# Kernel tuning notes

Measured on AMD Instinct MI355X. Metric: run time of the kernel, lower is better.

## Reference

```python
import jax, jax.numpy as jnp
import numpy as np

HEADS = 16
D_MODEL = 1024


def setup_inputs() -> dict:
    key = jax.random.key(0)
    ks = jax.random.split(key, 12)
    B, S, D = 4, 2048, D_MODEL
    s = 1.0 / np.sqrt(D)
    return {
        "q": jax.random.normal(ks[0], (B, S, D), jnp.float32),
        "k": jax.random.normal(ks[1], (B, S, D), jnp.float32),
        "v": jax.random.normal(ks[2], (B, S, D), jnp.float32),
        "mask": jnp.ones((B, S, S), jnp.int32),
        "W_q": jax.random.normal(ks[3], (D, D), jnp.float32) * s,
        "b_q": jnp.zeros((D,), jnp.float32),
        "W_k": jax.random.normal(ks[4], (D, D), jnp.float32) * s,
        "b_k": jnp.zeros((D,), jnp.float32),
        "W_v": jax.random.normal(ks[5], (D, D), jnp.float32) * s,
        "b_v": jnp.zeros((D,), jnp.float32),
        "W_o": jax.random.normal(ks[6], (D, D), jnp.float32) * s,
        "b_o": jnp.zeros((D,), jnp.float32),
    }


def reference(q, k, v, mask, W_q, b_q, W_k, b_k, W_v, b_v, W_o, b_o):
    B, Sq, D = q.shape
    H = HEADS
    d_k = D // H
    # torch Linear: x @ W.T + b
    qh = (q @ W_q.T + b_q).reshape(B, Sq, H, d_k).transpose(0, 2, 1, 3)
    kh = (k @ W_k.T + b_k).reshape(B, -1, H, d_k).transpose(0, 2, 1, 3)
    vh = (v @ W_v.T + b_v).reshape(B, -1, H, d_k).transpose(0, 2, 1, 3)
    scores = jnp.einsum("bhqd,bhkd->bhqk", qh, kh) / jnp.sqrt(jnp.float32(d_k))
    scores = jnp.where(mask[:, None, :, :] == 0, -jnp.inf, scores)
    attn = jax.nn.softmax(scores, axis=-1)
    out = jnp.einsum("bhqk,bhkd->bhqd", attn, vh)
    out = out.transpose(0, 2, 1, 3).reshape(B, Sq, D)
    return out @ W_o.T + b_o
```

## Files before the change

### kernel.cpp

```cpp
#include <hip/hip_runtime.h>
#include <hip/hip_bf16.h>
#include <cmath>
#include <cstddef>

#define B_  4
#define S_  2048
#define D_  1024
#define H_  16
#define DK_ 64
#define M_  (B_*S_)
#define MB(x) ((size_t)(x) << 20)

typedef unsigned short u16;
typedef __attribute__((ext_vector_type(8))) short s16x8;
typedef __attribute__((ext_vector_type(8))) unsigned short u16x8;
typedef __attribute__((ext_vector_type(4))) unsigned short u16x4;
typedef __attribute__((ext_vector_type(4))) float f32x4;
typedef __attribute__((ext_vector_type(4))) unsigned int u32x4;
typedef __attribute__((ext_vector_type(2))) unsigned long long ull2;

typedef __attribute__((address_space(3))) char as3char;
typedef __attribute__((address_space(1))) const char as1char;

__device__ inline u16 f2bf(float f) {
  unsigned int u = __float_as_uint(f);
  u += 0x7fffu + ((u >> 16) & 1u);
  return (u16)(u >> 16);
}
__device__ inline float bf2f(u16 h) {
  return __uint_as_float(((unsigned int)h) << 16);
}

__global__ __launch_bounds__(256)
void pack_mask(const int* __restrict__ mask, unsigned long long* __restrict__ Mp)
{
  int w    = blockIdx.x * 4 + (threadIdx.x >> 6);
  int lane = threadIdx.x & 63;
  int m = mask[(size_t)w * 64 + lane];
  unsigned long long bits = __ballot(m != 0);
  if (lane == 0) Mp[w] = bits;
}

__global__ __launch_bounds__(256)
void split_w(const float* __restrict__ W, u16* __restrict__ hi,
             u16* __restrict__ lo)
{
  int i = (blockIdx.x * 256 + threadIdx.x) * 4;
  float4 x = *(const float4*)(W + i);
  float xs[4] = {x.x, x.y, x.z, x.w};
  u16x4 h, l;
#pragma unroll
  for (int e = 0; e < 4; ++e) {
    u16 hh = f2bf(xs[e]);
    h[e] = hh;
    l[e] = f2bf(xs[e] - bf2f(hh));
  }
  *(u16x4*)(hi + i) = h;
  *(u16x4*)(lo + i) = l;
}

__global__ __launch_bounds__(256)
void cvt3(const float* __restrict__ a, const float* __restrict__ b,
          const float* __restrict__ c, u16* __restrict__ oa,
          u16* __restrict__ ob, u16* __restrict__ oc)
{
  const float* src = blockIdx.z == 0 ? a : (blockIdx.z == 1 ? b : c);
  u16*         dst = blockIdx.z == 0 ? oa : (blockIdx.z == 1 ? ob : oc);
  int id = blockIdx.x * 256 + threadIdx.x;
  int m  = id >> 7;
  int k8 = (id & 127) << 3;
  const float* p = src + (size_t)m * 1024 + k8;
  float4 x0 = *(const float4*)p;
  float4 x1 = *(const float4*)(p + 4);
  u16x8 px;
  px[0]=f2bf(x0.x); px[1]=f2bf(x0.y); px[2]=f2bf(x0.z); px[3]=f2bf(x0.w);
  px[4]=f2bf(x1.x); px[5]=f2bf(x1.y); px[6]=f2bf(x1.z); px[7]=f2bf(x1.w);
  int row = m & 127, kk = k8 & 63;
  size_t byte = ((size_t)((m >> 7) * 16 + (k8 >> 6)) << 14)
              + (size_t)((row * 128 + (kk >> 3) * 16) ^ ((row & 7) << 4));
  *(u16x8*)((char*)dst + byte) = px;
}

template<int OH, int ODK>
__global__ __launch_bounds__(256)
void proj_gemm_t(const u16* __restrict__ Xb, const u16* __restrict__ Wb,
                 const float* __restrict__ bias, u16* __restrict__ out,
                 float scale)
{
  __shared__ __align__(16) u16 smem[16384];
  char* const sX = (char*)smem;
  char* const sW = (char*)smem + 16384;

  const int tid  = threadIdx.x;
  const int lane = tid & 63, wid = tid >> 6;
  const int l15  = lane & 15, l4 = lane >> 4;
  const int wm = (wid >> 1) * 64, wn = (wid & 1) * 64;
  const int mb = blockIdx.x, nb = blockIdx.y;

  f32x4 acc[4][4];
#pragma unroll
  for (int i = 0; i < 4; ++i)
#pragma unroll
    for (int j = 0; j < 4; ++j)
      acc[i][j] = f32x4{0.f, 0.f, 0.f, 0.f};

  const char* xsrc = (const char*)Xb + ((size_t)(mb * 16) << 14) + wid * 4096 + lane * 16;
  const char* wsrc = (const char*)Wb + ((size_t)(nb * 16) << 14) + wid * 4096 + lane * 16;

  for (int kb = 0; kb < 16; ++kb) {
#pragma unroll
    for (int i = 0; i < 4; ++i) {
      __builtin_amdgcn_global_load_lds((const as1char*)(xsrc + i * 1024),
                                       (as3char*)(sX + wid * 4096 + i * 1024), 16, 0, 0);
      __builtin_amdgcn_global_load_lds((const as1char*)(wsrc + i * 1024),
                                       (as3char*)(sW + wid * 4096 + i * 1024), 16, 0, 0);
    }
    xsrc += 16384; wsrc += 16384;
    __syncthreads();

#pragma unroll
    for (int kc = 0; kc < 2; ++kc) {
      s16x8 af[4], bf[4];
#pragma unroll
      for (int i = 0; i < 4; ++i) {
        int ar = wm + i * 16 + l15;
        af[i] = *(const s16x8*)(sX + ((ar * 128 + kc * 64 + l4 * 16) ^ ((ar & 7) << 4)));
        int br = wn + i * 16 + l15;
        bf[i] = *(const s16x8*)(sW + ((br * 128 + kc * 64 + l4 * 16) ^ ((br & 7) << 4)));
      }
#pragma unroll
      for (int i = 0; i < 4; ++i)
#pragma unroll
        for (int j = 0; j < 4; ++j)
          acc[i][j] = __builtin_amdgcn_mfma_f32_16x16x32_bf16(af[i], bf[j], acc[i][j], 0, 0, 0);
    }
    __syncthreads();
  }

  float bj[4];
#pragma unroll
  for (int j = 0; j < 4; ++j) bj[j] = bias[nb * 128 + wn + j * 16 + l15];

#pragma unroll
  for (int i = 0; i < 4; ++i) {
#pragma unroll
    for (int r = 0; r < 4; ++r) {
      int mm = mb * 128 + wm + i * 16 + l4 * 4 + r;
      int bb = mm >> 11, s = mm & (S_ - 1);
#pragma unroll
      for (int j = 0; j < 4; ++j) {
        int n = nb * 128 + wn + j * 16 + l15;
        int hh = n / ODK, d = n % ODK;
        out[(((size_t)bb * OH + hh) * S_ + s) * ODK + d] =
            f2bf((acc[i][j][r] + bj[j]) * scale);
      }
    }
  }
}

__global__ __launch_bounds__(256)
void proj_out_split(const u16* __restrict__ Xhi, const u16* __restrict__ Xlo,
                    const u16* __restrict__ Whi, const u16* __restrict__ Wlo,
                    const float* __restrict__ bias, float* __restrict__ out,
                    int M, int N, int K)
{
  __shared__ __align__(16) u16 smem[32768];
  char* const sXh = (char*)smem;
  char* const sXl = (char*)smem + 16384;
  char* const sWh = (char*)smem + 32768;
  char* const sWl = (char*)smem + 49152;

  const int tid  = threadIdx.x;
  const int lane = tid & 63, wid = tid >> 6;
  const int l15  = lane & 15, l4 = lane >> 4;
  const int wm = (wid >> 1) * 64, wn = (wid & 1) * 64;
  const int m0 = blockIdx.x * 128, n0 = blockIdx.y * 128;

  f32x4 acc[4][4];
#pragma unroll
  for (int i = 0; i < 4; ++i)
#pragma unroll
    for (int j = 0; j < 4; ++j)
      acc[i][j] = f32x4{0.f, 0.f, 0.f, 0.f};

  for (int k0 = 0; k0 < K; k0 += 64) {
    __syncthreads();
#pragma unroll
    for (int n = 0; n < 4; ++n) {
      int c   = tid + n * 256;
      int row = c >> 3;
      int k8  = (c & 7) * 8;
      int dst = (row * 128 + (c & 7) * 16) ^ ((row & 7) << 4);
      size_t xoff = (size_t)(m0 + row) * K + k0 + k8;
      size_t woff = (size_t)(n0 + row) * K + k0 + k8;
      *(u16x8*)(sXh + dst) = *(const u16x8*)(Xhi + xoff);
      *(u16x8*)(sXl + dst) = *(const u16x8*)(Xlo + xoff);
      *(u16x8*)(sWh + dst) = *(const u16x8*)(Whi + woff);
      *(u16x8*)(sWl + dst) = *(const u16x8*)(Wlo + woff);
    }
    __syncthreads();

#pragma unroll
    for (int kc = 0; kc < 2; ++kc) {
      s16x8 ah[4], al[4], bh[4], bl[4];
#pragma unroll
      for (int i = 0; i < 4; ++i) {
        int ar = wm + i * 16 + l15;
        int aoff = (ar * 128 + kc * 64 + l4 * 16) ^ ((ar & 7) << 4);
        ah[i] = *(const s16x8*)(sXh + aoff);
        al[i] = *(const s16x8*)(sXl + aoff);
        int br = wn + i * 16 + l15;
        int boff = (br * 128 + kc * 64 + l4 * 16) ^ ((br & 7) << 4);
        bh[i] = *(const s16x8*)(sWh + boff);
        bl[i] = *(const s16x8*)(sWl + boff);
      }
#pragma unroll
      for (int i = 0; i < 4; ++i)
#pragma unroll
        for (int j = 0; j < 4; ++j) {
          acc[i][j] = __builtin_amdgcn_mfma_f32_16x16x32_bf16(ah[i], bh[j], acc[i][j], 0, 0, 0);
          acc[i][j] = __builtin_amdgcn_mfma_f32_16x16x32_bf16(ah[i], bl[j], acc[i][j], 0, 0, 0);
          acc[i][j] = __builtin_amdgcn_mfma_f32_16x16x32_bf16(al[i], bh[j], acc[i][j], 0, 0, 0);
        }
    }
  }

  float bj[4];
#pragma unroll
  for (int j = 0; j < 4; ++j) bj[j] = bias[n0 + wn + j * 16 + l15];

#pragma unroll
  for (int i = 0; i < 4; ++i) {
#pragma unroll
    for (int r = 0; r < 4; ++r) {
      int mm = m0 + wm + i * 16 + l4 * 4 + r;
#pragma unroll
      for (int j = 0; j < 4; ++j) {
        int n = n0 + wn + j * 16 + l15;
        out[(size_t)mm * N + n] = acc[i][j][r] + bj[j];
      }
    }
  }
}

__global__ __launch_bounds__(512)
void flash_attn_mfma4(const u16* __restrict__ Qh, const u16* __restrict__ Kh,
                      const u16* __restrict__ Vh,
                      const unsigned long long* __restrict__ Mp,
                      u16* __restrict__ AOhi, u16* __restrict__ AOlo)
{
  __shared__ __align__(16) char smem[16896];
  char* const sK = smem;
  char* const sV = smem + 8192;

  const int tid  = threadIdx.x;
  const int lane = tid & 63, wid = tid >> 6;
  const int l15  = lane & 15, l4 = lane >> 4;

  const int bh = blockIdx.y;
  const int b  = bh >> 4, h = bh & 15;
  const int q0 = blockIdx.x * 128;
  const int qw = q0 + wid * 16;
  const int myq = qw + l15;

  const float L2E = 1.4426950408889634f;

  const u16* qbase = Qh + ((size_t)bh * S_ + myq) * DK_;
  s16x8 qf[2];
  qf[0] = *(const s16x8*)(qbase + l4 * 8);
  qf[1] = *(const s16x8*)(qbase + 32 + l4 * 8);

  const int srow = tid >> 3;
  const int sd8  = (tid & 7) * 8;
  const int kdst = (srow * 128 + (tid & 7) * 16) ^ ((srow & 7) << 4);
  const u16* kg = Kh + (size_t)bh * S_ * DK_ + (size_t)srow * DK_ + sd8;
  const u16* vg = Vh + (size_t)bh * S_ * DK_ + (size_t)srow * DK_ + sd8;

  const int kswz = (l15 & 7) << 4;
  const int kcol = l4 * 16;

  const unsigned long long* mrow = Mp + ((size_t)b * S_ + myq) * (S_ / 64);

  f32x4 o[4];
#pragma unroll
  for (int n = 0; n < 4; ++n) o[n] = f32x4{0.f, 0.f, 0.f, 0.f};
  float m_i = -INFINITY, l_i = 0.f;
  float ml2 = -1e30f * L2E;

  for (int t = 0; t < S_ / 64; ++t) {
    __syncthreads();
    *(u16x8*)(sK + kdst) = *(const u16x8*)(kg + (size_t)t * 64 * DK_);
    u16x8 vv = *(const u16x8*)(vg + (size_t)t * 64 * DK_);
#pragma unroll
    for (int e = 0; e < 8; ++e) {
      int d = sd8 + e;
      *(u16*)(sV + d * 136 + ((srow * 2) ^ (((d >> 3) & 7) << 4))) = (u16)vv[e];
    }
    unsigned long long mbits = mrow[t];
    __syncthreads();

    f32x4 sc[4];
#pragma unroll
    for (int n = 0; n < 4; ++n) {
      sc[n] = f32x4{0.f, 0.f, 0.f, 0.f};
#pragma unroll
      for (int kc = 0; kc < 2; ++kc) {
        int row = n * 16 + l15;
        s16x8 kf = *(const s16x8*)(sK + ((row * 128 + kc * 64 + kcol) ^ kswz));
        sc[n] = __builtin_amdgcn_mfma_f32_16x16x32_bf16(kf, qf[kc], sc[n], 0, 0, 0);
      }
    }

    float s[4][4];
    if (__all(mbits == 0xFFFFFFFFFFFFFFFFull)) {
#pragma unroll
      for (int n = 0; n < 4; ++n)
#pragma unroll
        for (int r = 0; r < 4; ++r) s[n][r] = sc[n][r];
    } else {
#pragma unroll
      for (int n = 0; n < 4; ++n) {
        unsigned mb2 = (unsigned)(mbits >> (n * 16 + l4 * 4)) & 15u;
#pragma unroll
        for (int r = 0; r < 4; ++r)
          s[n][r] = (mb2 >> r) & 1u ? sc[n][r] : -INFINITY;
      }
    }

    float mt = fmaxf(fmaxf(s[0][0], s[0][1]), fmaxf(s[0][2], s[0][3]));
#pragma unroll
    for (int n = 1; n < 4; ++n)
      mt = fmaxf(mt, fmaxf(fmaxf(s[n][0], s[n][1]), fmaxf(s[n][2], s[n][3])));
    mt = fmaxf(mt, __shfl_xor(mt, 16));
    mt = fmaxf(mt, __shfl_xor(mt, 32));

    if (!__all(mt - m_i <= 8.f)) {
      float mn = fmaxf(m_i, mt);
      float alpha = (m_i == -INFINITY) ? 0.f
                    : __builtin_amdgcn_exp2f((m_i - mn) * L2E);
      float ab[4];
#pragma unroll
      for (int r = 0; r < 4; ++r) ab[r] = __shfl(alpha, l4 * 4 + r);
#pragma unroll
      for (int n = 0; n < 4; ++n)
#pragma unroll
        for (int r = 0; r < 4; ++r) o[n][r] *= ab[r];
      l_i *= alpha;
      m_i = mn;
      ml2 = fmaxf(mn, -1e30f) * L2E;
    }

    float p[4][4];
    float rs = 0.f;
#pragma unroll
    for (int n = 0; n < 4; ++n)
#pragma unroll
      for (int r = 0; r < 4; ++r) {
        p[n][r] = __builtin_amdgcn_exp2f(fmaf(s[n][r], L2E, -ml2));
        rs += p[n][r];
      }
    rs += __shfl_xor(rs, 16);
    rs += __shfl_xor(rs, 32);
    l_i += rs;

    s16x8 pf[2];
#pragma unroll
    for (int kc = 0; kc < 2; ++kc) {
      unsigned r0, r1, r2, r3;
      asm("v_cvt_pk_bf16_f32 %0, %1, %2" : "=v"(r0) : "v"(p[2*kc][0]),   "v"(p[2*kc][1]));
      asm("v_cvt_pk_bf16_f32 %0, %1, %2" : "=v"(r1) : "v"(p[2*kc][2]),   "v"(p[2*kc][3]));
      asm("v_cvt_pk_bf16_f32 %0, %1, %2" : "=v"(r2) : "v"(p[2*kc+1][0]), "v"(p[2*kc+1][1]));
      asm("v_cvt_pk_bf16_f32 %0, %1, %2" : "=v"(r3) : "v"(p[2*kc+1][2]), "v"(p[2*kc+1][3]));
      u32x4 uu = {r0, r1, r2, r3};
      pf[kc] = __builtin_bit_cast(s16x8, uu);
    }

#pragma unroll
    for (int kc = 0; kc < 2; ++kc) {
      int k0b = kc * 64 + 8 * l4;
#pragma unroll
      for (int n = 0; n < 4; ++n) {
        int d    = n * 16 + l15;
        int rowb = d * 136;
        int swz  = ((d >> 3) & 7) << 4;
        ull2 uu;
        uu[0] = *(const unsigned long long*)(sV + rowb + (k0b ^ swz));
        uu[1] = *(const unsigned long long*)(sV + rowb + ((k0b + 32) ^ swz));
        s16x8 vf = __builtin_bit_cast(s16x8, uu);
        o[n] = __builtin_amdgcn_mfma_f32_16x16x32_bf16(pf[kc], vf, o[n], 0, 0, 0);
      }
    }
  }

  float linv[4];
#pragma unroll
  for (int r = 0; r < 4; ++r) {
    float lr = __shfl(l_i, l4 * 4 + r);
    linv[r] = lr > 0.f ? 1.f / lr : 0.f;
  }
#pragma unroll
  for (int n = 0; n < 4; ++n)
#pragma unroll
    for (int r = 0; r < 4; ++r) {
      float val = o[n][r] * linv[r];
      u16 hh = f2bf(val);
      size_t oa = ((size_t)b * S_ + qw + l4 * 4 + r) * D_ + h * 64 + n * 16 + l15;
      AOhi[oa] = hh;
      AOlo[oa] = f2bf(val - bf2f(hh));
    }
}

extern "C" void kernel_launch(void* const* d_in, const int* in_sizes, int n_in,
                              void* d_out, int out_size, void* d_ws, size_t ws_size,
                              hipStream_t stream)
{
  const float* q    = (const float*)d_in[0];
  const float* k    = (const float*)d_in[1];
  const float* v    = (const float*)d_in[2];
  const int*   mask = (const int*)  d_in[3];
  const float* Wq   = (const float*)d_in[4];
  const float* bq   = (const float*)d_in[5];
  const float* Wk   = (const float*)d_in[6];
  const float* bk   = (const float*)d_in[7];
  const float* Wv   = (const float*)d_in[8];
  const float* bv   = (const float*)d_in[9];
  const float* Wo   = (const float*)d_in[10];
  const float* bo   = (const float*)d_in[11];
  float* out = (float*)d_out;

  char* ws = (char*)d_ws;
  u16* Qh   = (u16*)(ws);
  u16* Kh   = (u16*)(ws + MB(16));
  u16* Vh   = (u16*)(ws + MB(32));
  u16* AOhi = (u16*)(ws + MB(48));
  u16* AOlo = (u16*)(ws + MB(64));
  u16* Whi  = (u16*)(ws + MB(80));
  u16* Wlo  = (u16*)(ws + MB(82));
  unsigned long long* Mp = (unsigned long long*)(ws + MB(84));
  u16* kb2  = (u16*)(ws + MB(48));
  u16* qb2  = (u16*)(ws + MB(64));
  u16* vb2  = (u16*)(ws + MB(86));
  u16* Wqb  = (u16*)(ws + MB(102));
  u16* Wkb  = (u16*)(ws + MB(104));
  u16* Wvb  = (u16*)(ws + MB(106));

  dim3 tblk(256);

  cvt3<<<dim3(4096, 1, 3), tblk, 0, stream>>>(q, k, v, qb2, kb2, vb2);
  cvt3<<<dim3(512, 1, 3), tblk, 0, stream>>>(Wq, Wk, Wv, Wqb, Wkb, Wvb);
  pack_mask<<<dim3((B_ * S_ * (S_ / 64)) / 4), tblk, 0, stream>>>(mask, Mp);
  split_w<<<dim3((D_ * D_) / 1024), tblk, 0, stream>>>(Wo, Whi, Wlo);

  dim3 gproj(M_ / 128, D_ / 128);
  proj_gemm_t<H_, DK_><<<gproj, tblk, 0, stream>>>(qb2, Wqb, bq, Qh, 0.125f);
  proj_gemm_t<H_, DK_><<<gproj, tblk, 0, stream>>>(kb2, Wkb, bk, Kh, 1.0f);
  proj_gemm_t<H_, DK_><<<gproj, tblk, 0, stream>>>(vb2, Wvb, bv, Vh, 1.0f);

  dim3 gattn(S_ / 128, B_ * H_);
  flash_attn_mfma4<<<gattn, dim3(512), 0, stream>>>(Qh, Kh, Vh, Mp, AOhi, AOlo);

  proj_out_split<<<gproj, tblk, 0, stream>>>(AOhi, AOlo, Whi, Wlo, bo, out,
                                             M_, D_, D_);
}
```

Baseline: 317.3 us.

## Pre-tile operands, transpose V, and prefetch K/V tiles in attention

The V projection now writes a head-transposed layout (d-major), so the attention kernel can store V into shared memory with one vector write per thread instead of eight scalar transposing writes. The attention kernel also register-prefetches the next K/V tile and mask word. The attention output and the split Wo are written in the pre-swizzled tiled layout, so the output projection can load tiles straight into LDS with global_load_lds. The cost is scattered 2-byte stores in the attention epilogue and the V projection epilogue, plus an extra barrier per k-step in the output GEMM.

Result: faster. 301.1 us (-5.1%).

```diff
diff --git a/kernel.cpp b/kernel.cpp
--- a/kernel.cpp
+++ b/kernel.cpp
@@ -31,6 +31,12 @@
   return __uint_as_float(((unsigned int)h) << 16);
 }
 
+__device__ inline size_t tsw(int m, int k) {
+  int row = m & 127, kk = k & 63;
+  return ((size_t)((m >> 7) * 16 + (k >> 6)) << 14)
+       + (size_t)(((row * 128 + (kk >> 3) * 16) ^ ((row & 7) << 4)) + (kk & 7) * 2);
+}
+
 __global__ __launch_bounds__(256)
 void pack_mask(const int* __restrict__ mask, unsigned long long* __restrict__ Mp)
 {
@@ -42,21 +48,26 @@
 }
 
 __global__ __launch_bounds__(256)
-void split_w(const float* __restrict__ W, u16* __restrict__ hi,
-             u16* __restrict__ lo)
-{
-  int i = (blockIdx.x * 256 + threadIdx.x) * 4;
-  float4 x = *(const float4*)(W + i);
-  float xs[4] = {x.x, x.y, x.z, x.w};
-  u16x4 h, l;
-#pragma unroll
-  for (int e = 0; e < 4; ++e) {
+void split_w_t(const float* __restrict__ W, u16* __restrict__ hi,
+               u16* __restrict__ lo)
+{
+  int id = blockIdx.x * 256 + threadIdx.x;
+  int n  = id >> 7;
+  int k8 = (id & 127) << 3;
+  const float* p = W + (size_t)n * 1024 + k8;
+  float4 x0 = *(const float4*)p;
+  float4 x1 = *(const float4*)(p + 4);
+  float xs[8] = {x0.x, x0.y, x0.z, x0.w, x1.x, x1.y, x1.z, x1.w};
+  u16x8 h, l;
+#pragma unroll
+  for (int e = 0; e < 8; ++e) {
     u16 hh = f2bf(xs[e]);
     h[e] = hh;
     l[e] = f2bf(xs[e] - bf2f(hh));
   }
-  *(u16x4*)(hi + i) = h;
-  *(u16x4*)(lo + i) = l;
+  size_t byte = tsw(n, k8);
+  *(u16x8*)((char*)hi + byte) = h;
+  *(u16x8*)((char*)lo + byte) = l;
 }
 
 __global__ __launch_bounds__(256)
@@ -75,13 +86,10 @@
   u16x8 px;
   px[0]=f2bf(x0.x); px[1]=f2bf(x0.y); px[2]=f2bf(x0.z); px[3]=f2bf(x0.w);
   px[4]=f2bf(x1.x); px[5]=f2bf(x1.y); px[6]=f2bf(x1.z); px[7]=f2bf(x1.w);
-  int row = m & 127, kk = k8 & 63;
-  size_t byte = ((size_t)((m >> 7) * 16 + (k8 >> 6)) << 14)
-              + (size_t)((row * 128 + (kk >> 3) * 16) ^ ((row & 7) << 4));
-  *(u16x8*)((char*)dst + byte) = px;
-}
-
-template<int OH, int ODK>
+  *(u16x8*)((char*)dst + tsw(m, k8)) = px;
+}
+
+template<int MODE>
 __global__ __launch_bounds__(256)
 void proj_gemm_t(const u16* __restrict__ Xb, const u16* __restrict__ Wb,
                  const float* __restrict__ bias, u16* __restrict__ out,
@@ -150,19 +158,21 @@
 #pragma unroll
       for (int j = 0; j < 4; ++j) {
         int n = nb * 128 + wn + j * 16 + l15;
-        int hh = n / ODK, d = n % ODK;
-        out[(((size_t)bb * OH + hh) * S_ + s) * ODK + d] =
-            f2bf((acc[i][j][r] + bj[j]) * scale);
+        int hh = n >> 6, d = n & 63;
+        u16 val = f2bf((acc[i][j][r] + bj[j]) * scale);
+        if (MODE == 0)
+          out[(((size_t)bb * H_ + hh) * S_ + s) * DK_ + d] = val;
+        else
+          out[(((size_t)bb * H_ + hh) * DK_ + d) * S_ + s] = val;
       }
     }
   }
 }
 
 __global__ __launch_bounds__(256)
-void proj_out_split(const u16* __restrict__ Xhi, const u16* __restrict__ Xlo,
-                    const u16* __restrict__ Whi, const u16* __restrict__ Wlo,
-                    const float* __restrict__ bias, float* __restrict__ out,
-                    int M, int N, int K)
+void proj_out_t(const u16* __restrict__ Xhi, const u16* __restrict__ Xlo,
+                const u16* __restrict__ Whi, const u16* __restrict__ Wlo,
+                const float* __restrict__ bias, float* __restrict__ out)
 {
   __shared__ __align__(16) u16 smem[32768];
   char* const sXh = (char*)smem;
@@ -174,7 +184,7 @@
   const int lane = tid & 63, wid = tid >> 6;
   const int l15  = lane & 15, l4 = lane >> 4;
   const int wm = (wid >> 1) * 64, wn = (wid & 1) * 64;
-  const int m0 = blockIdx.x * 128, n0 = blockIdx.y * 128;
+  const int mb = blockIdx.x, nb = blockIdx.y;
 
   f32x4 acc[4][4];
 #pragma unroll
@@ -183,21 +193,25 @@
     for (int j = 0; j < 4; ++j)
       acc[i][j] = f32x4{0.f, 0.f, 0.f, 0.f};
 
-  for (int k0 = 0; k0 < K; k0 += 64) {
-    __syncthreads();
-#pragma unroll
-    for (int n = 0; n < 4; ++n) {
-      int c   = tid + n * 256;
-      int row = c >> 3;
-      int k8  = (c & 7) * 8;
-      int dst = (row * 128 + (c & 7) * 16) ^ ((row & 7) << 4);
-      size_t xoff = (size_t)(m0 + row) * K + k0 + k8;
-      size_t woff = (size_t)(n0 + row) * K + k0 + k8;
-      *(u16x8*)(sXh + dst) = *(const u16x8*)(Xhi + xoff);
-      *(u16x8*)(sXl + dst) = *(const u16x8*)(Xlo + xoff);
-      *(u16x8*)(sWh + dst) = *(const u16x8*)(Whi + woff);
-      *(u16x8*)(sWl + dst) = *(const u16x8*)(Wlo + woff);
-    }
+  const int toff = wid * 4096 + lane * 16;
+  const char* xh = (const char*)Xhi + ((size_t)(mb * 16) << 14) + toff;
+  const char* xl = (const char*)Xlo + ((size_t)(mb * 16) << 14) + toff;
+  const char* wh = (const char*)Whi + ((size_t)(nb * 16) << 14) + toff;
+  const char* wl = (const char*)Wlo + ((size_t)(nb * 16) << 14) + toff;
+
+  for (int kb = 0; kb < 16; ++kb) {
+#pragma unroll
+    for (int i = 0; i < 4; ++i) {
+      __builtin_amdgcn_global_load_lds((const as1char*)(xh + i * 1024),
+                                       (as3char*)(sXh + wid * 4096 + i * 1024), 16, 0, 0);
+      __builtin_amdgcn_global_load_lds((const as1char*)(xl + i * 1024),
+                                       (as3char*)(sXl + wid * 4096 + i * 1024), 16, 0, 0);
+      __builtin_amdgcn_global_load_lds((const as1char*)(wh + i * 1024),
+                                       (as3char*)(sWh + wid * 4096 + i * 1024), 16, 0, 0);
+      __builtin_amdgcn_global_load_lds((const as1char*)(wl + i * 1024),
+                                       (as3char*)(sWl + wid * 4096 + i * 1024), 16, 0, 0);
+    }
+    xh += 16384; xl += 16384; wh += 16384; wl += 16384;
     __syncthreads();
 
 #pragma unroll
@@ -223,29 +237,30 @@
           acc[i][j] = __builtin_amdgcn_mfma_f32_16x16x32_bf16(al[i], bh[j], acc[i][j], 0, 0, 0);
         }
     }
+    __syncthreads();
   }
 
   float bj[4];
 #pragma unroll
-  for (int j = 0; j < 4; ++j) bj[j] = bias[n0 + wn + j * 16 + l15];
+  for (int j = 0; j < 4; ++j) bj[j] = bias[nb * 128 + wn + j * 16 + l15];
 
 #pragma unroll
   for (int i = 0; i < 4; ++i) {
 #pragma unroll
     for (int r = 0; r < 4; ++r) {
-      int mm = m0 + wm + i * 16 + l4 * 4 + r;
+      int mm = mb * 128 + wm + i * 16 + l4 * 4 + r;
 #pragma unroll
       for (int j = 0; j < 4; ++j) {
-        int n = n0 + wn + j * 16 + l15;
-        out[(size_t)mm * N + n] = acc[i][j][r] + bj[j];
+        int n = nb * 128 + wn + j * 16 + l15;
+        out[(size_t)mm * D_ + n] = acc[i][j][r] + bj[j];
       }
     }
   }
 }
 
 __global__ __launch_bounds__(512)
-void flash_attn_mfma4(const u16* __restrict__ Qh, const u16* __restrict__ Kh,
-                      const u16* __restrict__ Vh,
+void flash_attn_mfma5(const u16* __restrict__ Qh, const u16* __restrict__ Kh,
+                      const u16* __restrict__ Vt,
                       const unsigned long long* __restrict__ Mp,
                       u16* __restrict__ AOhi, u16* __restrict__ AOlo)
 {
@@ -273,8 +288,9 @@
   const int srow = tid >> 3;
   const int sd8  = (tid & 7) * 8;
   const int kdst = (srow * 128 + (tid & 7) * 16) ^ ((srow & 7) << 4);
+  const int vdst = srow * 136 + (((tid & 7) * 16) ^ (((srow >> 3) & 7) << 4));
   const u16* kg = Kh + (size_t)bh * S_ * DK_ + (size_t)srow * DK_ + sd8;
-  const u16* vg = Vh + (size_t)bh * S_ * DK_ + (size_t)srow * DK_ + sd8;
+  const u16* vg = Vt + (size_t)bh * DK_ * S_ + (size_t)srow * S_ + sd8;
 
   const int kswz = (l15 & 7) << 4;
   const int kcol = l4 * 16;
@@ -287,17 +303,22 @@
   float m_i = -INFINITY, l_i = 0.f;
   float ml2 = -1e30f * L2E;
 
+  u16x8 kreg = *(const u16x8*)(kg);
+  u16x8 vreg = *(const u16x8*)(vg);
+  unsigned long long mb_next = mrow[0];
+
   for (int t = 0; t < S_ / 64; ++t) {
     __syncthreads();
-    *(u16x8*)(sK + kdst) = *(const u16x8*)(kg + (size_t)t * 64 * DK_);
-    u16x8 vv = *(const u16x8*)(vg + (size_t)t * 64 * DK_);
-#pragma unroll
-    for (int e = 0; e < 8; ++e) {
-      int d = sd8 + e;
-      *(u16*)(sV + d * 136 + ((srow * 2) ^ (((d >> 3) & 7) << 4))) = (u16)vv[e];
-    }
-    unsigned long long mbits = mrow[t];
-    __syncthreads();
+    *(u16x8*)(sK + kdst) = kreg;
+    *(u16x8*)(sV + vdst) = vreg;
+    unsigned long long mbits = mb_next;
+    __syncthreads();
+
+    if (t + 1 < S_ / 64) {
+      kreg = *(const u16x8*)(kg + (size_t)(t + 1) * 64 * DK_);
+      vreg = *(const u16x8*)(vg + (size_t)(t + 1) * 64);
+      mb_next = mrow[t + 1];
+    }
 
     f32x4 sc[4];
 #pragma unroll
@@ -404,9 +425,11 @@
     for (int r = 0; r < 4; ++r) {
       float val = o[n][r] * linv[r];
       u16 hh = f2bf(val);
-      size_t oa = ((size_t)b * S_ + qw + l4 * 4 + r) * D_ + h * 64 + n * 16 + l15;
-      AOhi[oa] = hh;
-      AOlo[oa] = f2bf(val - bf2f(hh));
+      int m = b * S_ + qw + l4 * 4 + r;
+      int k = h * 64 + n * 16 + l15;
+      size_t byte = tsw(m, k);
+      *(u16*)((char*)AOhi + byte) = hh;
+      *(u16*)((char*)AOlo + byte) = f2bf(val - bf2f(hh));
     }
 }
 
@@ -431,7 +454,7 @@
   char* ws = (char*)d_ws;
   u16* Qh   = (u16*)(ws);
   u16* Kh   = (u16*)(ws + MB(16));
-  u16* Vh   = (u16*)(ws + MB(32));
+  u16* Vt   = (u16*)(ws + MB(32));
   u16* AOhi = (u16*)(ws + MB(48));
   u16* AOlo = (u16*)(ws + MB(64));
   u16* Whi  = (u16*)(ws + MB(80));
@@ -449,16 +472,15 @@
   cvt3<<<dim3(4096, 1, 3), tblk, 0, stream>>>(q, k, v, qb2, kb2, vb2);
   cvt3<<<dim3(512, 1, 3), tblk, 0, stream>>>(Wq, Wk, Wv, Wqb, Wkb, Wvb);
   pack_mask<<<dim3((B_ * S_ * (S_ / 64)) / 4), tblk, 0, stream>>>(mask, Mp);
-  split_w<<<dim3((D_ * D_) / 1024), tblk, 0, stream>>>(Wo, Whi, Wlo);
+  split_w_t<<<dim3(512), tblk, 0, stream>>>(Wo, Whi, Wlo);
 
   dim3 gproj(M_ / 128, D_ / 128);
-  proj_gemm_t<H_, DK_><<<gproj, tblk, 0, stream>>>(qb2, Wqb, bq, Qh, 0.125f);
-  proj_gemm_t<H_, DK_><<<gproj, tblk, 0, stream>>>(kb2, Wkb, bk, Kh, 1.0f);
-  proj_gemm_t<H_, DK_><<<gproj, tblk, 0, stream>>>(vb2, Wvb, bv, Vh, 1.0f);
+  proj_gemm_t<0><<<gproj, tblk, 0, stream>>>(qb2, Wqb, bq, Qh, 0.125f);
+  proj_gemm_t<0><<<gproj, tblk, 0, stream>>>(kb2, Wkb, bk, Kh, 1.0f);
+  proj_gemm_t<1><<<gproj, tblk, 0, stream>>>(vb2, Wvb, bv, Vt, 1.0f);
 
   dim3 gattn(S_ / 128, B_ * H_);
-  flash_attn_mfma4<<<gattn, dim3(512), 0, stream>>>(Qh, Kh, Vh, Mp, AOhi, AOlo);
-
-  proj_out_split<<<gproj, tblk, 0, stream>>>(AOhi, AOlo, Whi, Wlo, bo, out,
-                                             M_, D_, D_);
-}
+  flash_attn_mfma5<<<gattn, dim3(512), 0, stream>>>(Qh, Kh, Vt, Mp, AOhi, AOlo);
+
+  proj_out_t<<<gproj, tblk, 0, stream>>>(AOhi, AOlo, Whi, Wlo, bo, out);
+}
```
